# Optimization experiments

Measured on AMD Instinct MI355X. Metric: run time of the kernel, lower is better.

The kernel has to match this reference:

```python
import jax, jax.numpy as jnp
import numpy as np

EMBED_DIM = 768
FF_DIM = 3072
NUM_EXPERTS = 8
TOP_K = 2
CAPACITY_FACTOR = 1.25  # training-mode capacity factor
LB_WEIGHT = 0.01
Z_WEIGHT = 0.001


def setup_inputs() -> dict:
    key = jax.random.key(0)
    k0, k1, k2, k3, k4 = jax.random.split(key, 5)
    B, S, D, F, E = 4, 2048, EMBED_DIM, FF_DIM, NUM_EXPERTS
    scale_d = 1.0 / np.sqrt(D)
    scale_f = 1.0 / np.sqrt(F)
    return {
        "x": jax.random.normal(k0, (B, S, D), dtype=jnp.float32),
        # router gate: nn.Linear(D, E, bias=False) -> weight [E, D]
        "w_gate": jax.random.normal(k1, (E, D), dtype=jnp.float32) * scale_d,
        # stacked expert weights, torch Linear layout [out, in]
        "wi_gate": jax.random.normal(k2, (E, F, D), dtype=jnp.float32) * scale_d,
        "wi_up": jax.random.normal(k3, (E, F, D), dtype=jnp.float32) * scale_d,
        "wo": jax.random.normal(k4, (E, D, F), dtype=jnp.float32) * scale_f,
    }


def moe_forward(x, w_gate, wi_gate, wi_up, wo):
    B, S, D = x.shape
    E = w_gate.shape[0]
    K = TOP_K
    T = B * S
    capacity = max(int(T * K / E * CAPACITY_FACTOR), K)

    xf = x.reshape(T, D)
    router_logits = xf @ w_gate.T                        # [T, E]
    router_probs = jax.nn.softmax(router_logits, axis=-1)
    topk_probs, topk_idx = jax.lax.top_k(router_probs, K)  # [T, K]
    topk_probs = topk_probs / topk_probs.sum(axis=-1, keepdims=True)

    # one-hot dispatch mask [T, K, E]
    onehot = (topk_idx[:, :, None] == jnp.arange(E)[None, None, :]).astype(xf.dtype)
    # per-(k, expert) arrival rank of each token (torch truncates first `capacity`
    # tokens in token-index order, independently per k and per expert)
    rank = ((jnp.cumsum(onehot, axis=0) - onehot) * onehot).sum(-1)  # [T, K]
    keep = (rank < capacity).astype(xf.dtype)                        # [T, K]

    # combine weights per (token, expert) [T, E]
    combine = jnp.einsum('tk,tk,tke->te', topk_probs, keep, onehot)

    out = jnp.zeros_like(xf)
    for e in range(E):  # fixed small structural loop over experts
        gate = jax.nn.silu(xf @ wi_gate[e].T)   # [T, F]
        up = xf @ wi_up[e].T                    # [T, F]
        y = (gate * up) @ wo[e].T               # [T, D]
        out = out + y * combine[:, e:e + 1]

    # auxiliary losses
    expert_mask = onehot.sum(axis=1)            # [T, E]
    f = expert_mask.sum(axis=0) / (T * K)
    P = router_probs.mean(axis=0)
    load_balance_loss = E * (f * P).sum()
    z_loss = jnp.mean(jax.nn.logsumexp(router_logits, axis=-1) ** 2)
    aux_loss = LB_WEIGHT * load_balance_loss + Z_WEIGHT * z_loss

    return out.reshape(B, S, D), aux_loss


def reference(x, w_gate, wi_gate, wi_up, wo):
    return moe_forward(x, w_gate, wi_gate, wi_up, wo)
```

## Files before the change

### kernel.cpp

```cpp
#include <hip/hip_runtime.h>

typedef unsigned short u16;
typedef unsigned int u32;
typedef unsigned long long u64;

#define T_TOK 8192
#define DIM 768
#define FF 3072
#define NE 8
#define CAP 2560
#define LSTR 5120
#define MAXMT 20

typedef __attribute__((ext_vector_type(8))) short s8v;
typedef __attribute__((ext_vector_type(4))) float f4v;

__device__ __forceinline__ u16 f2bf(float f) {
  union { float f; u32 u; } v; v.f = f;
  u32 r = v.u + 0x7FFFu + ((v.u >> 16) & 1u);
  return (u16)(r >> 16);
}

__device__ __forceinline__ void glds16(const void* g, void* l) {
  __builtin_amdgcn_global_load_lds(
      (const __attribute__((address_space(1))) u32*)g,
      (__attribute__((address_space(3))) u32*)l, 16, 0, 0);
}

__global__ __launch_bounds__(256) void cast3_kernel(
    const float* __restrict__ s0, const float* __restrict__ s1, const float* __restrict__ s2,
    u16* __restrict__ d0, u16* __restrict__ d1, u16* __restrict__ d2, int n8each) {
  int i = blockIdx.x * 256 + threadIdx.x;
  const float* s; u16* d; int j;
  if (i < n8each) { s = s0; d = d0; j = i; }
  else if (i < 2 * n8each) { s = s1; d = d1; j = i - n8each; }
  else { s = s2; d = d2; j = i - 2 * n8each; }
  const float4* s4 = (const float4*)s;
  float4 a = s4[2 * j], b = s4[2 * j + 1];
  uint4 o;
  o.x = (u32)f2bf(a.x) | ((u32)f2bf(a.y) << 16);
  o.y = (u32)f2bf(a.z) | ((u32)f2bf(a.w) << 16);
  o.z = (u32)f2bf(b.x) | ((u32)f2bf(b.y) << 16);
  o.w = (u32)f2bf(b.z) | ((u32)f2bf(b.w) << 16);
  ((uint4*)d)[j] = o;
}

__global__ __launch_bounds__(256) void router_kernel(
    const float* __restrict__ x, const float* __restrict__ wg, u16* __restrict__ xb,
    int* __restrict__ tki, float* __restrict__ tkp,
    float* __restrict__ probs, float* __restrict__ lse2) {
  int lane = threadIdx.x & 63;
  int t = blockIdx.x * 4 + (threadIdx.x >> 6);
  const float* xr = x + (long)t * DIM;
  u16* xw = xb + (long)t * DIM;
  float acc[NE];
#pragma unroll
  for (int e = 0; e < NE; e++) acc[e] = 0.f;
  for (int i = 0; i < DIM / 64; i++) {
    float xv = xr[lane + 64 * i];
    xw[lane + 64 * i] = f2bf(xv);
#pragma unroll
    for (int e = 0; e < NE; e++) acc[e] += xv * wg[e * DIM + lane + 64 * i];
  }
#pragma unroll
  for (int off = 32; off > 0; off >>= 1) {
#pragma unroll
    for (int e = 0; e < NE; e++) acc[e] += __shfl_xor(acc[e], off);
  }
  if (lane == 0) {
    float m = acc[0];
#pragma unroll
    for (int e = 1; e < NE; e++) m = fmaxf(m, acc[e]);
    float p[NE], s = 0.f;
#pragma unroll
    for (int e = 0; e < NE; e++) { p[e] = __expf(acc[e] - m); s += p[e]; }
    float inv = 1.f / s;
    int e0 = 0;
#pragma unroll
    for (int e = 1; e < NE; e++) if (acc[e] > acc[e0]) e0 = e;
    int e1 = (e0 == 0) ? 1 : 0;
#pragma unroll
    for (int e = 0; e < NE; e++) if (e != e0 && acc[e] > acc[e1]) e1 = e;
    float p0 = p[e0] * inv, p1 = p[e1] * inv;
    float rn = 1.f / (p0 + p1);
    tki[2 * t] = e0; tki[2 * t + 1] = e1;
    tkp[2 * t] = p0 * rn; tkp[2 * t + 1] = p1 * rn;
    float4 pa = {p[0] * inv, p[1] * inv, p[2] * inv, p[3] * inv};
    float4 pb = {p[4] * inv, p[5] * inv, p[6] * inv, p[7] * inv};
    ((float4*)(probs + t * 8))[0] = pa;
    ((float4*)(probs + t * 8))[1] = pb;
    float lse = __logf(s) + m;
    lse2[t] = lse * lse;
  }
}

__global__ __launch_bounds__(1024) void reduce_router_kernel(
    const int* __restrict__ tki, const float* __restrict__ probs, const float* __restrict__ lse2,
    int* __restrict__ fcnt, float* __restrict__ psum, float* __restrict__ zsum) {
  int t = blockIdx.x * 1024 + threadIdx.x;
  float4 pa = ((const float4*)(probs + t * 8))[0];
  float4 pb = ((const float4*)(probs + t * 8))[1];
  float p[8] = {pa.x, pa.y, pa.z, pa.w, pb.x, pb.y, pb.z, pb.w};
  float z = lse2[t];
  int e0 = tki[2 * t], e1 = tki[2 * t + 1];
  int fc[8];
#pragma unroll
  for (int e = 0; e < 8; e++) fc[e] = (e0 == e ? 1 : 0) + (e1 == e ? 1 : 0);
#pragma unroll
  for (int off = 32; off > 0; off >>= 1) {
#pragma unroll
    for (int e = 0; e < 8; e++) { p[e] += __shfl_xor(p[e], off); fc[e] += __shfl_xor(fc[e], off); }
    z += __shfl_xor(z, off);
  }
  __shared__ float sp[16][9];
  __shared__ int sf[16][8];
  int wv = threadIdx.x >> 6, lane = threadIdx.x & 63;
  if (lane == 0) {
#pragma unroll
    for (int e = 0; e < 8; e++) { sp[wv][e] = p[e]; sf[wv][e] = fc[e]; }
    sp[wv][8] = z;
  }
  __syncthreads();
  if (threadIdx.x < 9) {
    float s = 0.f;
    for (int w = 0; w < 16; w++) s += sp[w][threadIdx.x];
    if (threadIdx.x < 8) atomicAdd(&psum[threadIdx.x], s);
    else atomicAdd(zsum, s);
  }
  if (threadIdx.x >= 64 && threadIdx.x < 72) {
    int e = threadIdx.x - 64;
    int s = 0;
    for (int w = 0; w < 16; w++) s += sf[w][e];
    atomicAdd(&fcnt[e], s);
  }
}

__global__ __launch_bounds__(1024) void rank_dispatch_kernel(
    const int* __restrict__ tki, const float* __restrict__ tkp,
    int* __restrict__ ltk, float* __restrict__ lw,
    int* __restrict__ counts, int* __restrict__ baserow, int* __restrict__ kflags) {
  __shared__ int wave_cnt[2][16][8];
  __shared__ int base[2][8];
  __shared__ int sc0[8];
  int tid = threadIdx.x, wv = tid >> 6, lane = tid & 63;
  int c0w[8];
#pragma unroll
  for (int e = 0; e < 8; e++) c0w[e] = 0;
  for (int c = 0; c < T_TOK / 1024; c++) {
    int e0 = tki[2 * (c * 1024 + tid)];
#pragma unroll
    for (int e = 0; e < 8; e++) {
      u64 m = __ballot(e0 == e);
      if (lane == 0) c0w[e] += __popcll(m);
    }
  }
  if (lane == 0) {
#pragma unroll
    for (int e = 0; e < 8; e++) wave_cnt[0][wv][e] = c0w[e];
  }
  if (tid < 16) base[tid >> 3][tid & 7] = 0;
  __syncthreads();
  if (tid < 8) {
    int s = 0;
    for (int w = 0; w < 16; w++) s += wave_cnt[0][w][tid];
    sc0[tid] = (s < CAP) ? s : CAP;
  }
  __syncthreads();
  u64 lmask = (lane == 63) ? 0x7FFFFFFFFFFFFFFFull : ((1ull << lane) - 1ull);
  for (int c = 0; c < T_TOK / 1024; c++) {
    int t = c * 1024 + tid;
    int e0 = tki[2 * t], e1 = tki[2 * t + 1];
    float p0 = tkp[2 * t], p1 = tkp[2 * t + 1];
    int pre0 = 0, pre1 = 0;
    for (int e = 0; e < 8; e++) {
      u64 m0 = __ballot(e0 == e);
      if (e0 == e) pre0 = __popcll(m0 & lmask);
      if (lane == 0) wave_cnt[0][wv][e] = __popcll(m0);
      u64 m1 = __ballot(e1 == e);
      if (e1 == e) pre1 = __popcll(m1 & lmask);
      if (lane == 0) wave_cnt[1][wv][e] = __popcll(m1);
    }
    __syncthreads();
    if (tid < 16) {
      int k = tid >> 3, e = tid & 7;
      int run = base[k][e];
      for (int w = 0; w < 16; w++) {
        int v = wave_cnt[k][w][e];
        wave_cnt[k][w][e] = run;
        run += v;
      }
      base[k][e] = run;
    }
    __syncthreads();
    int r0 = wave_cnt[0][wv][e0] + pre0;
    int r1 = wave_cnt[1][wv][e1] + pre1;
    if (r0 < CAP) { ltk[e0 * LSTR + r0] = (t << 1); lw[e0 * LSTR + r0] = p0; }
    if (r1 < CAP) {
      int p = sc0[e1] + r1;
      ltk[e1 * LSTR + p] = (t << 1) | 1; lw[e1 * LSTR + p] = p1;
    }
    kflags[t] = (r0 < CAP ? 1 : 0) | (r1 < CAP ? 2 : 0);
    __syncthreads();
  }
  if (tid == 0) {
    int run = 0;
    for (int e = 0; e < 8; e++) {
      int c1 = base[1][e]; if (c1 > CAP) c1 = CAP;
      int cnt = sc0[e] + c1;
      counts[e] = cnt; baserow[e] = run; run += cnt;
    }
  }
}

__global__ __launch_bounds__(256, 2) void gemm1_kernel(
    const u16* __restrict__ xb, const u16* __restrict__ wgb, const u16* __restrict__ wub,
    u16* __restrict__ H, const int* __restrict__ counts, const int* __restrict__ baserow,
    const int* __restrict__ ltk) {
  int id = blockIdx.x;
  int xcd = id & 7;
  int q = id >> 3;
  int gg = q / MAXMT;
  int mt = q - gg * MAXMT;
  int g = gg * 8 + xcd;
  int e = g / 48;
  int nt = g - e * 48;
  int cnt = counts[e];
  if (mt * 128 >= cnt) return;

  __shared__ u16 As[128 * 64];
  __shared__ u16 Bg[64 * 64];
  __shared__ u16 Bu[64 * 64];
  __shared__ int toks[128];
  int tid = threadIdx.x;
  if (tid < 128) {
    int r = mt * 128 + tid; if (r > cnt - 1) r = cnt - 1;
    toks[tid] = ltk[e * LSTR + r] >> 1;
  }
  __syncthreads();
  int rq8 = tid >> 3;
  int swz = ((tid & 7) ^ (rq8 & 7)) * 8;
  long tA0 = toks[rq8], tA1 = toks[32 + rq8], tA2 = toks[64 + rq8], tA3 = toks[96 + rq8];
  const u16* gA0 = xb + tA0 * DIM + swz;
  const u16* gA1 = xb + tA1 * DIM + swz;
  const u16* gA2 = xb + tA2 * DIM + swz;
  const u16* gA3 = xb + tA3 * DIM + swz;
  long bO0 = ((long)e * FF + nt * 64 + rq8) * DIM + swz;
  long bO1 = bO0 + 32l * DIM;
  const u16* gG0 = wgb + bO0; const u16* gG1 = wgb + bO1;
  const u16* gU0 = wub + bO0; const u16* gU1 = wub + bO1;
  u16* dA0 = As + tid * 8; u16* dA1 = dA0 + 2048; u16* dA2 = dA0 + 4096; u16* dA3 = dA0 + 6144;
  u16* dG0 = Bg + tid * 8; u16* dG1 = dG0 + 2048;
  u16* dU0 = Bu + tid * 8; u16* dU1 = dU0 + 2048;

  int lane = tid & 63, wv = tid >> 6;
  int wm = (wv & 1) * 64, wn = (wv >> 1) * 32;
  int lrow = lane & 15, quad = lane >> 4;
  int sl0 = (quad ^ (lrow & 7)) * 8;
  int sl1 = ((quad + 4) ^ (lrow & 7)) * 8;

  f4v zero = {0.f, 0.f, 0.f, 0.f};
  f4v accg[4][2], accu[4][2];
#pragma unroll
  for (int i = 0; i < 4; i++)
#pragma unroll
    for (int j = 0; j < 2; j++) { accg[i][j] = zero; accu[i][j] = zero; }

  for (int kt = 0; kt < DIM / 64; kt++) {
    int ko = kt * 64;
    __syncthreads();
    glds16(gA0 + ko, dA0); glds16(gA1 + ko, dA1);
    glds16(gA2 + ko, dA2); glds16(gA3 + ko, dA3);
    glds16(gG0 + ko, dG0); glds16(gG1 + ko, dG1);
    glds16(gU0 + ko, dU0); glds16(gU1 + ko, dU1);
    __syncthreads();
#pragma unroll
    for (int kk = 0; kk < 2; kk++) {
      int sl = kk ? sl1 : sl0;
      s8v a[4], bgf[2], buf[2];
#pragma unroll
      for (int i = 0; i < 4; i++)
        a[i] = *(const s8v*)&As[(wm + i * 16 + lrow) * 64 + sl];
#pragma unroll
      for (int j = 0; j < 2; j++) {
        bgf[j] = *(const s8v*)&Bg[(wn + j * 16 + lrow) * 64 + sl];
        buf[j] = *(const s8v*)&Bu[(wn + j * 16 + lrow) * 64 + sl];
      }
#pragma unroll
      for (int i = 0; i < 4; i++)
#pragma unroll
        for (int j = 0; j < 2; j++) {
          accg[i][j] = __builtin_amdgcn_mfma_f32_16x16x32_bf16(a[i], bgf[j], accg[i][j], 0, 0, 0);
          accu[i][j] = __builtin_amdgcn_mfma_f32_16x16x32_bf16(a[i], buf[j], accu[i][j], 0, 0, 0);
        }
    }
  }
  long hb = (long)baserow[e] + (long)mt * 128;
#pragma unroll
  for (int i = 0; i < 4; i++) {
#pragma unroll
    for (int r = 0; r < 4; r++) {
      int m = wm + i * 16 + quad * 4 + r;
      if (mt * 128 + m < cnt) {
#pragma unroll
        for (int j = 0; j < 2; j++) {
          float gv = accg[i][j][r], uv = accu[i][j][r];
          float h = gv / (1.f + __expf(-gv)) * uv;
          H[(hb + m) * FF + nt * 64 + wn + j * 16 + lrow] = f2bf(h);
        }
      }
    }
  }
}

__global__ __launch_bounds__(256, 2) void gemm2_kernel(
    const u16* __restrict__ H, const u16* __restrict__ wob,
    float* __restrict__ ybuf, const int* __restrict__ counts, const int* __restrict__ baserow,
    const int* __restrict__ ltk, const float* __restrict__ lw) {
  int id = blockIdx.x;
  int xcd = id & 7;
  int q = id >> 3;
  int gg = q / 6;
  int nt = q - gg * 6;
  int g = gg * 8 + xcd;
  int e = g / MAXMT;
  int mt = g - e * MAXMT;
  int cnt = counts[e];
  if (mt * 128 >= cnt) return;

  __shared__ u16 As[128 * 64];
  __shared__ u16 Bs[128 * 64];
  __shared__ int stok[128];
  __shared__ float sw[128];
  int tid = threadIdx.x;
  if (tid < 128) {
    int r = mt * 128 + tid; if (r > cnt - 1) r = cnt - 1;
    stok[tid] = ltk[e * LSTR + r];
    sw[tid] = lw[e * LSTR + r];
  }
  long hb = (long)baserow[e] + (long)mt * 128;
  int rq8 = tid >> 3;
  int swz = ((tid & 7) ^ (rq8 & 7)) * 8;
  const u16* gA0 = H + (hb + rq8) * FF + swz;
  const u16* gA1 = gA0 + 32l * FF;
  const u16* gA2 = gA0 + 64l * FF;
  const u16* gA3 = gA0 + 96l * FF;
  long bOff = ((long)e * DIM + nt * 128 + rq8) * FF + swz;
  const u16* gB0 = wob + bOff;
  const u16* gB1 = gB0 + 32l * FF;
  const u16* gB2 = gB0 + 64l * FF;
  const u16* gB3 = gB0 + 96l * FF;
  u16* dA0 = As + tid * 8; u16* dA1 = dA0 + 2048; u16* dA2 = dA0 + 4096; u16* dA3 = dA0 + 6144;
  u16* dB0 = Bs + tid * 8; u16* dB1 = dB0 + 2048; u16* dB2 = dB0 + 4096; u16* dB3 = dB0 + 6144;
  int lane = tid & 63, wv = tid >> 6;
  int wm = (wv & 1) * 64, wn = (wv >> 1) * 64;
  int lrow = lane & 15, quad = lane >> 4;
  int sl0 = (quad ^ (lrow & 7)) * 8;
  int sl1 = ((quad + 4) ^ (lrow & 7)) * 8;
  f4v zero = {0.f, 0.f, 0.f, 0.f};
  f4v acc[4][4];
#pragma unroll
  for (int i = 0; i < 4; i++)
#pragma unroll
    for (int j = 0; j < 4; j++) acc[i][j] = zero;

  for (int kt = 0; kt < FF / 64; kt++) {
    int ko = kt * 64;
    __syncthreads();
    glds16(gA0 + ko, dA0); glds16(gA1 + ko, dA1);
    glds16(gA2 + ko, dA2); glds16(gA3 + ko, dA3);
    glds16(gB0 + ko, dB0); glds16(gB1 + ko, dB1);
    glds16(gB2 + ko, dB2); glds16(gB3 + ko, dB3);
    __syncthreads();
#pragma unroll
    for (int kk = 0; kk < 2; kk++) {
      int sl = kk ? sl1 : sl0;
      s8v a[4], b[4];
#pragma unroll
      for (int i = 0; i < 4; i++)
        a[i] = *(const s8v*)&As[(wm + i * 16 + lrow) * 64 + sl];
#pragma unroll
      for (int j = 0; j < 4; j++)
        b[j] = *(const s8v*)&Bs[(wn + j * 16 + lrow) * 64 + sl];
#pragma unroll
      for (int i = 0; i < 4; i++)
#pragma unroll
        for (int j = 0; j < 4; j++)
          acc[i][j] = __builtin_amdgcn_mfma_f32_16x16x32_bf16(a[i], b[j], acc[i][j], 0, 0, 0);
    }
  }
#pragma unroll
  for (int i = 0; i < 4; i++) {
#pragma unroll
    for (int r = 0; r < 4; r++) {
      int m = wm + i * 16 + quad * 4 + r;
      if (mt * 128 + m < cnt) {
        int entry = stok[m];
        float w = sw[m];
        long ob = (long)entry * DIM + nt * 128;
#pragma unroll
        for (int j = 0; j < 4; j++)
          ybuf[ob + wn + j * 16 + lrow] = acc[i][j][r] * w;
      }
    }
  }
}

__global__ __launch_bounds__(256) void combine_kernel(
    const float* __restrict__ ybuf, const int* __restrict__ kflags, float* __restrict__ out) {
  int idx = blockIdx.x * 256 + threadIdx.x;
  int t = idx / (DIM / 4);
  int d4 = idx - t * (DIM / 4);
  int kf = kflags[t];
  float4 r = {0.f, 0.f, 0.f, 0.f};
  if (kf & 1) {
    float4 a = ((const float4*)(ybuf + (long)(2 * t) * DIM))[d4];
    r.x += a.x; r.y += a.y; r.z += a.z; r.w += a.w;
  }
  if (kf & 2) {
    float4 b = ((const float4*)(ybuf + (long)(2 * t + 1) * DIM))[d4];
    r.x += b.x; r.y += b.y; r.z += b.z; r.w += b.w;
  }
  ((float4*)out)[idx] = r;
}

__global__ void aux_kernel(const int* __restrict__ fcnt, const float* __restrict__ psum,
                           const float* __restrict__ zsum, float* __restrict__ outaux) {
  if (threadIdx.x == 0 && blockIdx.x == 0) {
    float lb = 0.f;
    for (int e = 0; e < 8; e++)
      lb += ((float)fcnt[e] / (float)(T_TOK * 2)) * (psum[e] / (float)T_TOK);
    lb *= 8.f;
    float z = zsum[0] / (float)T_TOK;
    outaux[0] = 0.01f * lb + 0.001f * z;
  }
}

extern "C" void kernel_launch(void* const* d_in, const int* in_sizes, int n_in,
                              void* d_out, int out_size, void* d_ws, size_t ws_size,
                              hipStream_t stream) {
  const float* x = (const float*)d_in[0];
  const float* wgate = (const float*)d_in[1];
  const float* wig = (const float*)d_in[2];
  const float* wiu = (const float*)d_in[3];
  const float* wo = (const float*)d_in[4];
  float* out = (float*)d_out;

  char* ws = (char*)d_ws;
  size_t off = 0;
  auto alloc = [&](size_t bytes) {
    void* p = ws + off;
    off += (bytes + 255) & ~(size_t)255;
    return p;
  };
  int* ctrl = (int*)alloc(256);
  u16* xb = (u16*)alloc((size_t)T_TOK * DIM * 2);
  u16* wgb = (u16*)alloc((size_t)NE * FF * DIM * 2);
  u16* wub = (u16*)alloc((size_t)NE * FF * DIM * 2);
  u16* wob = (u16*)alloc((size_t)NE * DIM * FF * 2);
  u16* Hbuf = (u16*)alloc((size_t)(T_TOK * 2 + 128) * FF * 2);
  int* tki = (int*)alloc((size_t)T_TOK * 2 * 4);
  float* tkp = (float*)alloc((size_t)T_TOK * 2 * 4);
  int* ltk = (int*)alloc((size_t)NE * LSTR * 4);
  float* lw = (float*)alloc((size_t)NE * LSTR * 4);
  float* probs = (float*)alloc((size_t)T_TOK * 8 * 4);
  float* lse2 = (float*)alloc((size_t)T_TOK * 4);
  int* kflags = (int*)alloc((size_t)T_TOK * 4);
  float* ybuf = (float*)wgb;

  int* fcnt = ctrl;
  int* counts = ctrl + 8;
  int* baserow = ctrl + 16;
  float* psum = (float*)(ctrl + 24);
  float* zsum = (float*)(ctrl + 32);

  const int n8each = NE * FF * DIM / 8;
  hipMemsetAsync(ctrl, 0, 256, stream);
  cast3_kernel<<<3 * n8each / 256, 256, 0, stream>>>(wig, wiu, wo, wgb, wub, wob, n8each);
  router_kernel<<<T_TOK / 4, 256, 0, stream>>>(x, wgate, xb, tki, tkp, probs, lse2);
  reduce_router_kernel<<<T_TOK / 1024, 1024, 0, stream>>>(tki, probs, lse2, fcnt, psum, zsum);
  rank_dispatch_kernel<<<1, 1024, 0, stream>>>(tki, tkp, ltk, lw, counts, baserow, kflags);
  gemm1_kernel<<<8 * 48 * MAXMT, 256, 0, stream>>>(xb, wgb, wub, Hbuf, counts, baserow, ltk);
  gemm2_kernel<<<8 * MAXMT * 6, 256, 0, stream>>>(Hbuf, wob, ybuf, counts, baserow, ltk, lw);
  combine_kernel<<<T_TOK * DIM / 4 / 256, 256, 0, stream>>>(ybuf, kflags, out);
  aux_kernel<<<1, 64, 0, stream>>>(fcnt, psum, zsum, out + (size_t)T_TOK * DIM);
}
```

Before: 582.7 us.

## Rewrite expert GEMMs as 256x256 double-buffered 8-wave pipelined tiles

Both expert GEMM kernels move from 128-row tiles with a single LDS buffer and two barriers per k-step to 256x256 tiles run by 512 threads. LDS is double-buffered and global-to-LDS loads are interleaved with four MFMA quadrants, using explicit vmcnt waits and s_setprio. The gate and up weight rows are interleaved into a single B tile so one accumulator set holds both. The goal is to hide memory latency behind compute and raise arithmetic intensity per tile. The cost is a large LDS footprint (128KB), more register pressure, and fewer workgroups for gemm2, which may leave CUs underused.

Result: slower. 666.2 us (+14.3%).

```diff
diff --git a/kernel.cpp b/kernel.cpp
--- a/kernel.cpp
+++ b/kernel.cpp
@@ -10,7 +10,6 @@
 #define NE 8
 #define CAP 2560
 #define LSTR 5120
-#define MAXMT 20
 
 typedef __attribute__((ext_vector_type(8))) short s8v;
 typedef __attribute__((ext_vector_type(4))) float f4v;
@@ -26,6 +25,12 @@
       (const __attribute__((address_space(1))) u32*)g,
       (__attribute__((address_space(3))) u32*)l, 16, 0, 0);
 }
+
+#define BARRIER() do { asm volatile("" ::: "memory"); __builtin_amdgcn_s_barrier(); asm volatile("" ::: "memory"); } while (0)
+#define WAITV(N) asm volatile("s_waitcnt vmcnt(" #N ")" ::: "memory")
+#define WAITL() asm volatile("s_waitcnt lgkmcnt(0)" ::: "memory")
+#define PRIO1 __builtin_amdgcn_s_setprio(1)
+#define PRIO0 __builtin_amdgcn_s_setprio(0)
 
 __global__ __launch_bounds__(256) void cast3_kernel(
     const float* __restrict__ s0, const float* __restrict__ s1, const float* __restrict__ s2,
@@ -212,197 +217,241 @@
   }
 }
 
-__global__ __launch_bounds__(256, 2) void gemm1_kernel(
+#define LOADA(MS, PB) \
+  _Pragma("unroll") for (int i_ = 0; i_ < 4; i_++) { \
+    const u16* rp_ = (PB) + ((MS) * 64 + i_ * 16 + lrow) * 64; \
+    a[i_][0] = *(const s8v*)(rp_ + sx0); \
+    a[i_][1] = *(const s8v*)(rp_ + sx1); }
+#define LOADB(DST, NS, PB) \
+  _Pragma("unroll") for (int j_ = 0; j_ < 2; j_++) { \
+    const u16* rp_ = (PB) + (cb + (NS) * 32 + j_ * 16 + lrow) * 64; \
+    DST[j_][0] = *(const s8v*)(rp_ + sx0); \
+    DST[j_][1] = *(const s8v*)(rp_ + sx1); }
+#define QMFMA(MS, NS, BREG) \
+  _Pragma("unroll") for (int i_ = 0; i_ < 4; i_++) { \
+    _Pragma("unroll") for (int j_ = 0; j_ < 2; j_++) { \
+      acc[(MS) * 4 + i_][(NS) * 2 + j_] = __builtin_amdgcn_mfma_f32_16x16x32_bf16( \
+          a[i_][0], BREG[j_][0], acc[(MS) * 4 + i_][(NS) * 2 + j_], 0, 0, 0); \
+      acc[(MS) * 4 + i_][(NS) * 2 + j_] = __builtin_amdgcn_mfma_f32_16x16x32_bf16( \
+          a[i_][1], BREG[j_][1], acc[(MS) * 4 + i_][(NS) * 2 + j_], 0, 0, 0); } }
+
+__global__ __launch_bounds__(512, 2) void gemm1_kernel(
     const u16* __restrict__ xb, const u16* __restrict__ wgb, const u16* __restrict__ wub,
     u16* __restrict__ H, const int* __restrict__ counts, const int* __restrict__ baserow,
     const int* __restrict__ ltk) {
   int id = blockIdx.x;
-  int xcd = id & 7;
-  int q = id >> 3;
-  int gg = q / MAXMT;
-  int mt = q - gg * MAXMT;
-  int g = gg * 8 + xcd;
-  int e = g / 48;
-  int nt = g - e * 48;
+  int wgi = (id & 7) * 240 + (id >> 3);
+  int e = wgi / 240;
+  int rem = wgi - e * 240;
+  int NT = rem / 10;
+  int mt = rem - NT * 10;
   int cnt = counts[e];
-  if (mt * 128 >= cnt) return;
-
-  __shared__ u16 As[128 * 64];
-  __shared__ u16 Bg[64 * 64];
-  __shared__ u16 Bu[64 * 64];
-  __shared__ int toks[128];
+  if (mt * 256 >= cnt) return;
+
+  __shared__ u16 A[2][2][128 * 64];
+  __shared__ u16 B[2][2][128 * 64];
+  __shared__ int toks[256];
   int tid = threadIdx.x;
-  if (tid < 128) {
-    int r = mt * 128 + tid; if (r > cnt - 1) r = cnt - 1;
+  if (tid < 256) {
+    int r = mt * 256 + tid; if (r > cnt - 1) r = cnt - 1;
     toks[tid] = ltk[e * LSTR + r] >> 1;
   }
   __syncthreads();
-  int rq8 = tid >> 3;
-  int swz = ((tid & 7) ^ (rq8 & 7)) * 8;
-  long tA0 = toks[rq8], tA1 = toks[32 + rq8], tA2 = toks[64 + rq8], tA3 = toks[96 + rq8];
-  const u16* gA0 = xb + tA0 * DIM + swz;
-  const u16* gA1 = xb + tA1 * DIM + swz;
-  const u16* gA2 = xb + tA2 * DIM + swz;
-  const u16* gA3 = xb + tA3 * DIM + swz;
-  long bO0 = ((long)e * FF + nt * 64 + rq8) * DIM + swz;
-  long bO1 = bO0 + 32l * DIM;
-  const u16* gG0 = wgb + bO0; const u16* gG1 = wgb + bO1;
-  const u16* gU0 = wub + bO0; const u16* gU1 = wub + bO1;
-  u16* dA0 = As + tid * 8; u16* dA1 = dA0 + 2048; u16* dA2 = dA0 + 4096; u16* dA3 = dA0 + 6144;
-  u16* dG0 = Bg + tid * 8; u16* dG1 = dG0 + 2048;
-  u16* dU0 = Bu + tid * 8; u16* dU1 = dU0 + 2048;
+
+#define STAGE_A1(P, H_, KT) do { \
+    int S_ = tid; \
+    _Pragma("unroll") for (int c_ = 0; c_ < 2; c_++, S_ += 512) { \
+      int row_ = S_ >> 3; int l_ = (S_ & 7) ^ (row_ & 7); \
+      glds16(xb + (long)toks[(H_) * 128 + row_] * DIM + (KT) * 64 + l_ * 8, \
+             &A[P][H_][S_ * 8]); \
+    } } while (0)
+#define STAGE_B1(P, H_, KT) do { \
+    int S_ = tid; \
+    _Pragma("unroll") for (int c_ = 0; c_ < 2; c_++, S_ += 512) { \
+      int row_ = S_ >> 3; int l_ = (S_ & 7) ^ (row_ & 7); \
+      int rr_ = NT * 256 + (H_) * 128 + row_; \
+      int f_ = ((rr_ >> 5) << 4) + (rr_ & 15); \
+      const u16* bs_ = ((rr_ >> 4) & 1) ? wub : wgb; \
+      glds16(bs_ + ((long)e * FF + f_) * DIM + (KT) * 64 + l_ * 8, \
+             &B[P][H_][S_ * 8]); \
+    } } while (0)
 
   int lane = tid & 63, wv = tid >> 6;
-  int wm = (wv & 1) * 64, wn = (wv >> 1) * 32;
+  int wm = (wv & 1) * 128;
+  int wn = (wv >> 1) * 64;
   int lrow = lane & 15, quad = lane >> 4;
-  int sl0 = (quad ^ (lrow & 7)) * 8;
-  int sl1 = ((quad + 4) ^ (lrow & 7)) * 8;
-
-  f4v zero = {0.f, 0.f, 0.f, 0.f};
-  f4v accg[4][2], accu[4][2];
-#pragma unroll
-  for (int i = 0; i < 4; i++)
-#pragma unroll
-    for (int j = 0; j < 2; j++) { accg[i][j] = zero; accu[i][j] = zero; }
-
-  for (int kt = 0; kt < DIM / 64; kt++) {
-    int ko = kt * 64;
-    __syncthreads();
-    glds16(gA0 + ko, dA0); glds16(gA1 + ko, dA1);
-    glds16(gA2 + ko, dA2); glds16(gA3 + ko, dA3);
-    glds16(gG0 + ko, dG0); glds16(gG1 + ko, dG1);
-    glds16(gU0 + ko, dU0); glds16(gU1 + ko, dU1);
-    __syncthreads();
-#pragma unroll
-    for (int kk = 0; kk < 2; kk++) {
-      int sl = kk ? sl1 : sl0;
-      s8v a[4], bgf[2], buf[2];
-#pragma unroll
-      for (int i = 0; i < 4; i++)
-        a[i] = *(const s8v*)&As[(wm + i * 16 + lrow) * 64 + sl];
-#pragma unroll
-      for (int j = 0; j < 2; j++) {
-        bgf[j] = *(const s8v*)&Bg[(wn + j * 16 + lrow) * 64 + sl];
-        buf[j] = *(const s8v*)&Bu[(wn + j * 16 + lrow) * 64 + sl];
-      }
-#pragma unroll
-      for (int i = 0; i < 4; i++)
-#pragma unroll
-        for (int j = 0; j < 2; j++) {
-          accg[i][j] = __builtin_amdgcn_mfma_f32_16x16x32_bf16(a[i], bgf[j], accg[i][j], 0, 0, 0);
-          accu[i][j] = __builtin_amdgcn_mfma_f32_16x16x32_bf16(a[i], buf[j], accu[i][j], 0, 0, 0);
-        }
-    }
-  }
-  long hb = (long)baserow[e] + (long)mt * 128;
-#pragma unroll
-  for (int i = 0; i < 4; i++) {
-#pragma unroll
-    for (int r = 0; r < 4; r++) {
-      int m = wm + i * 16 + quad * 4 + r;
-      if (mt * 128 + m < cnt) {
-#pragma unroll
-        for (int j = 0; j < 2; j++) {
-          float gv = accg[i][j][r], uv = accu[i][j][r];
+  int cb = wn & 64;
+  int sx0 = (quad ^ (lrow & 7)) * 8;
+  int sx1 = ((quad + 4) ^ (lrow & 7)) * 8;
+  const u16* Awb = &A[0][wm >> 7][0];
+  const u16* Bwb = &B[0][wn >> 7][0];
+
+  f4v acc[8][4];
+#pragma unroll
+  for (int i = 0; i < 8; i++)
+#pragma unroll
+    for (int j = 0; j < 4; j++) acc[i][j] = (f4v){0.f, 0.f, 0.f, 0.f};
+  s8v a[4][2], b0[2][2], b1[2][2];
+
+  STAGE_A1(0, 0, 0); STAGE_A1(0, 1, 0); STAGE_B1(0, 0, 0); STAGE_B1(0, 1, 0);
+  STAGE_B1(1, 0, 1); STAGE_A1(1, 0, 1);
+  WAITV(4);
+  BARRIER();
+
+  for (int kt = 0; kt < 12; kt++) {
+    int p = kt & 1;
+    const u16* Ap = Awb + p * (2 * 128 * 64);
+    const u16* Bp = Bwb + p * (2 * 128 * 64);
+    LOADA(0, Ap);
+    LOADB(b0, 0, Bp);
+    if (kt + 1 < 12) STAGE_A1(p ^ 1, 1, kt + 1);
+    BARRIER(); WAITL();
+    PRIO1; QMFMA(0, 0, b0); PRIO0;
+    BARRIER();
+    LOADB(b1, 1, Bp);
+    if (kt + 1 < 12) STAGE_B1(p ^ 1, 1, kt + 1);
+    BARRIER(); WAITL();
+    PRIO1; QMFMA(0, 1, b1); PRIO0;
+    BARRIER();
+    LOADA(1, Ap);
+    if (kt + 2 < 12) STAGE_B1(p, 0, kt + 2);
+    BARRIER(); WAITL();
+    PRIO1; QMFMA(1, 1, b1); PRIO0;
+    BARRIER();
+    if (kt + 2 < 12) STAGE_A1(p, 0, kt + 2);
+    if (kt < 10) { WAITV(4); } else { WAITV(0); }
+    BARRIER();
+    PRIO1; QMFMA(1, 0, b0); PRIO0;
+    BARRIER();
+  }
+
+  long hb = (long)baserow[e] + (long)mt * 256;
+#pragma unroll
+  for (int mi = 0; mi < 8; mi++) {
+#pragma unroll
+    for (int r4 = 0; r4 < 4; r4++) {
+      int m = wm + (mi >> 2) * 64 + (mi & 3) * 16 + quad * 4 + r4;
+      if (mt * 256 + m < cnt) {
+#pragma unroll
+        for (int pr = 0; pr < 2; pr++) {
+          float gv = acc[mi][pr * 2][r4], uv = acc[mi][pr * 2 + 1][r4];
           float h = gv / (1.f + __expf(-gv)) * uv;
-          H[(hb + m) * FF + nt * 64 + wn + j * 16 + lrow] = f2bf(h);
+          H[(hb + m) * FF + NT * 128 + (wn >> 1) + pr * 16 + lrow] = f2bf(h);
         }
       }
     }
   }
-}
-
-__global__ __launch_bounds__(256, 2) void gemm2_kernel(
-    const u16* __restrict__ H, const u16* __restrict__ wob,
+#undef STAGE_A1
+#undef STAGE_B1
+}
+
+__global__ __launch_bounds__(512, 2) void gemm2_kernel(
+    const u16* __restrict__ Hsrc, const u16* __restrict__ wob,
     float* __restrict__ ybuf, const int* __restrict__ counts, const int* __restrict__ baserow,
     const int* __restrict__ ltk, const float* __restrict__ lw) {
   int id = blockIdx.x;
-  int xcd = id & 7;
-  int q = id >> 3;
-  int gg = q / 6;
-  int nt = q - gg * 6;
-  int g = gg * 8 + xcd;
-  int e = g / MAXMT;
-  int mt = g - e * MAXMT;
+  int wgi = (id & 7) * 30 + (id >> 3);
+  int e = wgi / 30;
+  int rem = wgi - e * 30;
+  int mt = rem / 3;
+  int nt = rem - mt * 3;
   int cnt = counts[e];
-  if (mt * 128 >= cnt) return;
-
-  __shared__ u16 As[128 * 64];
-  __shared__ u16 Bs[128 * 64];
-  __shared__ int stok[128];
-  __shared__ float sw[128];
+  if (mt * 256 >= cnt) return;
+
+  __shared__ u16 A[2][2][128 * 64];
+  __shared__ u16 B[2][2][128 * 64];
+  __shared__ int stok[256];
+  __shared__ float sw[256];
   int tid = threadIdx.x;
-  if (tid < 128) {
-    int r = mt * 128 + tid; if (r > cnt - 1) r = cnt - 1;
+  if (tid < 256) {
+    int r = mt * 256 + tid; if (r > cnt - 1) r = cnt - 1;
     stok[tid] = ltk[e * LSTR + r];
     sw[tid] = lw[e * LSTR + r];
   }
-  long hb = (long)baserow[e] + (long)mt * 128;
-  int rq8 = tid >> 3;
-  int swz = ((tid & 7) ^ (rq8 & 7)) * 8;
-  const u16* gA0 = H + (hb + rq8) * FF + swz;
-  const u16* gA1 = gA0 + 32l * FF;
-  const u16* gA2 = gA0 + 64l * FF;
-  const u16* gA3 = gA0 + 96l * FF;
-  long bOff = ((long)e * DIM + nt * 128 + rq8) * FF + swz;
-  const u16* gB0 = wob + bOff;
-  const u16* gB1 = gB0 + 32l * FF;
-  const u16* gB2 = gB0 + 64l * FF;
-  const u16* gB3 = gB0 + 96l * FF;
-  u16* dA0 = As + tid * 8; u16* dA1 = dA0 + 2048; u16* dA2 = dA0 + 4096; u16* dA3 = dA0 + 6144;
-  u16* dB0 = Bs + tid * 8; u16* dB1 = dB0 + 2048; u16* dB2 = dB0 + 4096; u16* dB3 = dB0 + 6144;
+  __syncthreads();
+  long hb0 = baserow[e];
+
+#define STAGE_A2(P, H_, KT) do { \
+    int S_ = tid; \
+    _Pragma("unroll") for (int c_ = 0; c_ < 2; c_++, S_ += 512) { \
+      int row_ = S_ >> 3; int l_ = (S_ & 7) ^ (row_ & 7); \
+      int r_ = mt * 256 + (H_) * 128 + row_; if (r_ > cnt - 1) r_ = cnt - 1; \
+      glds16(Hsrc + (hb0 + r_) * FF + (KT) * 64 + l_ * 8, &A[P][H_][S_ * 8]); \
+    } } while (0)
+#define STAGE_B2(P, H_, KT) do { \
+    int S_ = tid; \
+    _Pragma("unroll") for (int c_ = 0; c_ < 2; c_++, S_ += 512) { \
+      int row_ = S_ >> 3; int l_ = (S_ & 7) ^ (row_ & 7); \
+      glds16(wob + ((long)e * DIM + nt * 256 + (H_) * 128 + row_) * FF + (KT) * 64 + l_ * 8, \
+             &B[P][H_][S_ * 8]); \
+    } } while (0)
+
   int lane = tid & 63, wv = tid >> 6;
-  int wm = (wv & 1) * 64, wn = (wv >> 1) * 64;
+  int wm = (wv & 1) * 128;
+  int wn = (wv >> 1) * 64;
   int lrow = lane & 15, quad = lane >> 4;
-  int sl0 = (quad ^ (lrow & 7)) * 8;
-  int sl1 = ((quad + 4) ^ (lrow & 7)) * 8;
-  f4v zero = {0.f, 0.f, 0.f, 0.f};
-  f4v acc[4][4];
-#pragma unroll
-  for (int i = 0; i < 4; i++)
-#pragma unroll
-    for (int j = 0; j < 4; j++) acc[i][j] = zero;
-
-  for (int kt = 0; kt < FF / 64; kt++) {
-    int ko = kt * 64;
-    __syncthreads();
-    glds16(gA0 + ko, dA0); glds16(gA1 + ko, dA1);
-    glds16(gA2 + ko, dA2); glds16(gA3 + ko, dA3);
-    glds16(gB0 + ko, dB0); glds16(gB1 + ko, dB1);
-    glds16(gB2 + ko, dB2); glds16(gB3 + ko, dB3);
-    __syncthreads();
-#pragma unroll
-    for (int kk = 0; kk < 2; kk++) {
-      int sl = kk ? sl1 : sl0;
-      s8v a[4], b[4];
-#pragma unroll
-      for (int i = 0; i < 4; i++)
-        a[i] = *(const s8v*)&As[(wm + i * 16 + lrow) * 64 + sl];
-#pragma unroll
-      for (int j = 0; j < 4; j++)
-        b[j] = *(const s8v*)&Bs[(wn + j * 16 + lrow) * 64 + sl];
-#pragma unroll
-      for (int i = 0; i < 4; i++)
-#pragma unroll
-        for (int j = 0; j < 4; j++)
-          acc[i][j] = __builtin_amdgcn_mfma_f32_16x16x32_bf16(a[i], b[j], acc[i][j], 0, 0, 0);
-    }
-  }
-#pragma unroll
-  for (int i = 0; i < 4; i++) {
-#pragma unroll
-    for (int r = 0; r < 4; r++) {
-      int m = wm + i * 16 + quad * 4 + r;
-      if (mt * 128 + m < cnt) {
+  int cb = wn & 64;
+  int sx0 = (quad ^ (lrow & 7)) * 8;
+  int sx1 = ((quad + 4) ^ (lrow & 7)) * 8;
+  const u16* Awb = &A[0][wm >> 7][0];
+  const u16* Bwb = &B[0][wn >> 7][0];
+
+  f4v acc[8][4];
+#pragma unroll
+  for (int i = 0; i < 8; i++)
+#pragma unroll
+    for (int j = 0; j < 4; j++) acc[i][j] = (f4v){0.f, 0.f, 0.f, 0.f};
+  s8v a[4][2], b0[2][2], b1[2][2];
+
+  STAGE_A2(0, 0, 0); STAGE_A2(0, 1, 0); STAGE_B2(0, 0, 0); STAGE_B2(0, 1, 0);
+  STAGE_B2(1, 0, 1); STAGE_A2(1, 0, 1);
+  WAITV(4);
+  BARRIER();
+
+  for (int kt = 0; kt < 48; kt++) {
+    int p = kt & 1;
+    const u16* Ap = Awb + p * (2 * 128 * 64);
+    const u16* Bp = Bwb + p * (2 * 128 * 64);
+    LOADA(0, Ap);
+    LOADB(b0, 0, Bp);
+    if (kt + 1 < 48) STAGE_A2(p ^ 1, 1, kt + 1);
+    BARRIER(); WAITL();
+    PRIO1; QMFMA(0, 0, b0); PRIO0;
+    BARRIER();
+    LOADB(b1, 1, Bp);
+    if (kt + 1 < 48) STAGE_B2(p ^ 1, 1, kt + 1);
+    BARRIER(); WAITL();
+    PRIO1; QMFMA(0, 1, b1); PRIO0;
+    BARRIER();
+    LOADA(1, Ap);
+    if (kt + 2 < 48) STAGE_B2(p, 0, kt + 2);
+    BARRIER(); WAITL();
+    PRIO1; QMFMA(1, 1, b1); PRIO0;
+    BARRIER();
+    if (kt + 2 < 48) STAGE_A2(p, 0, kt + 2);
+    if (kt < 46) { WAITV(4); } else { WAITV(0); }
+    BARRIER();
+    PRIO1; QMFMA(1, 0, b0); PRIO0;
+    BARRIER();
+  }
+
+#pragma unroll
+  for (int mi = 0; mi < 8; mi++) {
+#pragma unroll
+    for (int r4 = 0; r4 < 4; r4++) {
+      int m = wm + (mi >> 2) * 64 + (mi & 3) * 16 + quad * 4 + r4;
+      if (mt * 256 + m < cnt) {
         int entry = stok[m];
         float w = sw[m];
-        long ob = (long)entry * DIM + nt * 128;
-#pragma unroll
-        for (int j = 0; j < 4; j++)
-          ybuf[ob + wn + j * 16 + lrow] = acc[i][j][r] * w;
+        long ob = (long)entry * DIM + nt * 256 + wn;
+#pragma unroll
+        for (int jc = 0; jc < 4; jc++)
+          ybuf[ob + jc * 16 + lrow] = acc[mi][jc][r4] * w;
       }
     }
   }
+#undef STAGE_A2
+#undef STAGE_B2
 }
 
 __global__ __launch_bounds__(256) void combine_kernel(
@@ -457,7 +506,7 @@
   u16* wgb = (u16*)alloc((size_t)NE * FF * DIM * 2);
   u16* wub = (u16*)alloc((size_t)NE * FF * DIM * 2);
   u16* wob = (u16*)alloc((size_t)NE * DIM * FF * 2);
-  u16* Hbuf = (u16*)alloc((size_t)(T_TOK * 2 + 128) * FF * 2);
+  u16* Hbuf = (u16*)alloc((size_t)(T_TOK * 2 + 256) * FF * 2);
   int* tki = (int*)alloc((size_t)T_TOK * 2 * 4);
   float* tkp = (float*)alloc((size_t)T_TOK * 2 * 4);
   int* ltk = (int*)alloc((size_t)NE * LSTR * 4);
@@ -479,8 +528,8 @@
   router_kernel<<<T_TOK / 4, 256, 0, stream>>>(x, wgate, xb, tki, tkp, probs, lse2);
   reduce_router_kernel<<<T_TOK / 1024, 1024, 0, stream>>>(tki, probs, lse2, fcnt, psum, zsum);
   rank_dispatch_kernel<<<1, 1024, 0, stream>>>(tki, tkp, ltk, lw, counts, baserow, kflags);
-  gemm1_kernel<<<8 * 48 * MAXMT, 256, 0, stream>>>(xb, wgb, wub, Hbuf, counts, baserow, ltk);
-  gemm2_kernel<<<8 * MAXMT * 6, 256, 0, stream>>>(Hbuf, wob, ybuf, counts, baserow, ltk, lw);
+  gemm1_kernel<<<1920, 512, 0, stream>>>(xb, wgb, wub, Hbuf, counts, baserow, ltk);
+  gemm2_kernel<<<240, 512, 0, stream>>>(Hbuf, wob, ybuf, counts, baserow, ltk, lw);
   combine_kernel<<<T_TOK * DIM / 4 / 256, 256, 0, stream>>>(ybuf, kflags, out);
   aux_kernel<<<1, 64, 0, stream>>>(fcnt, psum, zsum, out + (size_t)T_TOK * DIM);
 }
```
